# Performance work log

Hardware: AMD Instinct MI355X
Metric: run time of the kernel (lower is better)

## Reference

```python
import jax, jax.numpy as jnp
import numpy as np

N = 20000      # nodes
IN = 256       # in_dim
OUT = 128      # out_dim
S = 8          # num_sect
K = S + 1      # sectors + self branch
EP = 40000     # edges per sector


def setup_inputs() -> dict:
    key = jax.random.key(0)
    ks = jax.random.split(key, 10)
    x = jax.random.normal(ks[0], (N, IN), jnp.float32)
    rows = jax.random.randint(ks[1], (S, EP), 0, N)  # src (adj row)
    cols = jax.random.randint(ks[2], (S, EP), 0, N)  # dst (adj col)
    # degree norms (buffers derived from the graph, as in compute_norm)
    out_deg = np.bincount(np.asarray(rows).ravel(), minlength=N).astype(np.float32)
    in_deg = np.bincount(np.asarray(cols).ravel(), minlength=N).astype(np.float32)
    out_norm = jnp.asarray(np.clip(out_deg, 1.0, None) ** -0.5)[:, None]  # [N,1]
    in_norm = jnp.asarray(np.clip(in_deg, 1.0, None) ** -0.5)[:, None]    # [N,1]
    s = 0.05  # xavier-ish scale
    W_self = jax.random.normal(ks[3], (IN, OUT), jnp.float32) * s
    W_sect = jax.random.normal(ks[4], (S, IN, OUT), jnp.float32) * s
    WC = jax.random.normal(ks[5], (OUT, OUT), jnp.float32) * s
    WD = jax.random.normal(ks[6], (OUT, OUT), jnp.float32) * s
    gate_w = jax.random.normal(ks[7], (2 * K * OUT, 1), jnp.float32) * s
    gate_b = jnp.zeros((1,), jnp.float32)
    return {"x": x, "W_self": W_self, "W_sect": W_sect, "WC": WC, "WD": WD,
            "gate_w": gate_w, "gate_b": gate_b, "out_norm": out_norm,
            "in_norm": in_norm, "rows": rows, "cols": cols}


def reference(x, W_self, W_sect, WC, WD, gate_w, gate_b, out_norm, in_norm, rows, cols):
    n = x.shape[0]
    # --- forward_sector_agg (dropout is identity in eval / drop_rate=0) ---
    z_self = x @ W_self                                    # [N, OUT]
    H = jnp.einsum('ni,sio->sno', x, W_sect) * out_norm    # [S, N, OUT]
    def agg(h, r, c):  # sparse adj @ h : z[src] += h[dst]
        return jax.ops.segment_sum(h[c], r, num_segments=n)
    Z = jax.vmap(agg)(H, rows, cols)                       # [S, N, OUT]
    z = jnp.concatenate([z_self[None], Z], axis=0)         # [K, N, OUT]
    z = jnp.transpose(z, (1, 0, 2)) * in_norm[:, :, None]  # [N, K, OUT]
    # --- heter_sen_interaction ---
    zc = z @ WC                                            # [N, K, D]
    com = jnp.einsum('nkd,njd->nkj', zc, zc)
    ac = jax.nn.softmax(com, axis=2)
    z_com = jnp.einsum('nkj,njd->nkd', ac, zc).reshape(n, -1)
    zd = z @ WD
    sub = zd[:, :, None, :] - zd[:, None, :, :]            # [N, K, K, D]
    ds = jnp.einsum('nkd,nkjd->nkj', zd, sub)
    ad = jax.nn.softmax(ds, axis=2)
    z_dis = jnp.einsum('nkj,nkjd->nkd', ad, sub).reshape(n, -1)
    cat = jnp.concatenate([z_com, z_dis], axis=-1)         # [N, 2*K*D]
    beta = jax.nn.sigmoid(cat @ gate_w + gate_b)           # [N, 1]
    return beta * z_com + (1.0 - beta) * z_dis             # [N, K*D]
```

## Files before the change

### kernel.cpp

```cpp
#include <hip/hip_runtime.h>
#include <math.h>

#define N_NODES 20000
#define IN_DIM  256
#define OUT_DIM 128
#define S_SECT  8
#define K_BR    9
#define NK      (K_BR*OUT_DIM)
#define EP_EDGE 40000
#define N_EDGES (S_SECT*EP_EDGE)
#define N_BINS  (S_SECT*N_NODES)
#define SCAN_BLOCKS 160
#define M_ROWS  (N_NODES*K_BR)
#define BP      264
#define ZP      136

typedef float v4f __attribute__((ext_vector_type(4)));
typedef short v8s __attribute__((ext_vector_type(8)));

__device__ inline unsigned short f2bf(float f) {
  union { float f; unsigned u; } v; v.f = f;
  unsigned r = v.u + 0x7fff + ((v.u >> 16) & 1);
  return (unsigned short)(r >> 16);
}
__device__ inline float bf2f(unsigned short h) {
  union { unsigned u; float f; } v; v.u = ((unsigned)h) << 16;
  return v.f;
}

__global__ __launch_bounds__(256) void k_prep_wt(
    const float* __restrict__ Wself, const float* __restrict__ Wsect,
    unsigned short* __restrict__ Wtg)
{
  const int id = blockIdx.x * 256 + threadIdx.x;
  if (id >= NK*IN_DIM) return;
  const int j = id >> 8, k = id & 255;
  float w;
  if (j < OUT_DIM) w = Wself[(size_t)k*OUT_DIM + j];
  else {
    const int s = (j - OUT_DIM) >> 7, c = (j - OUT_DIM) & 127;
    w = Wsect[(size_t)s*(IN_DIM*OUT_DIM) + (size_t)k*OUT_DIM + c];
  }
  Wtg[id] = f2bf(w);
}

__global__ __launch_bounds__(256) void k_prep_xbf(
    const float* __restrict__ x, unsigned short* __restrict__ xbf)
{
  const int id = blockIdx.x * 256 + threadIdx.x;
  if (id >= N_NODES*IN_DIM/4) return;
  const float4 v = ((const float4*)x)[id];
  uint2 o;
  o.x = (unsigned)f2bf(v.x) | ((unsigned)f2bf(v.y) << 16);
  o.y = (unsigned)f2bf(v.z) | ((unsigned)f2bf(v.w) << 16);
  ((uint2*)xbf)[id] = o;
}

__global__ __launch_bounds__(256, 2) void k_gemm_xw_mfma(
    const unsigned short* __restrict__ xbf, const unsigned short* __restrict__ Wtg,
    const float* __restrict__ outn, const float* __restrict__ inn,
    unsigned short* __restrict__ Hbuf, unsigned short* __restrict__ Zbufh)
{
  __shared__ unsigned short Bls[128*BP];
  const int t = threadIdx.x;
  const int wave = t >> 6, lane = t & 63;
  const int mrow = lane & 15, quad = lane >> 4;
  const int m0 = blockIdx.x * 128 + wave * 32;
  const int jbase = blockIdx.y * 128;

  #pragma unroll
  for (int i = 0; i < 16; ++i) {
    const int idx = t + i*256;
    const int col = idx >> 5, ch = idx & 31;
    *(uint4*)(Bls + col*BP + ch*8) =
        *(const uint4*)(Wtg + (size_t)(jbase + col)*IN_DIM + ch*8);
  }

  v8s afr[2][8];
  #pragma unroll
  for (int rb = 0; rb < 2; ++rb) {
    const int r = m0 + rb*16 + mrow;
    const bool ok = (r < N_NODES);
    const unsigned short* src = xbf + (size_t)r*IN_DIM + quad*8;
    #pragma unroll
    for (int kq = 0; kq < 8; ++kq) {
      v8s f = {0,0,0,0,0,0,0,0};
      if (ok) f = *(const v8s*)(src + kq*32);
      afr[rb][kq] = f;
    }
  }
  __syncthreads();

  v4f acc[2][8];
  #pragma unroll
  for (int rb = 0; rb < 2; ++rb)
    #pragma unroll
    for (int jt = 0; jt < 8; ++jt) acc[rb][jt] = (v4f){0.f,0.f,0.f,0.f};

  #pragma unroll
  for (int kq = 0; kq < 8; ++kq) {
    #pragma unroll
    for (int jt = 0; jt < 8; ++jt) {
      const v8s bf = *(const v8s*)(Bls + (jt*16 + mrow)*BP + kq*32 + quad*8);
      acc[0][jt] = __builtin_amdgcn_mfma_f32_16x16x32_bf16(afr[0][kq], bf, acc[0][jt], 0, 0, 0);
      acc[1][jt] = __builtin_amdgcn_mfma_f32_16x16x32_bf16(afr[1][kq], bf, acc[1][jt], 0, 0, 0);
    }
  }

  if (blockIdx.y == 0) {
    #pragma unroll
    for (int rb = 0; rb < 2; ++rb)
      #pragma unroll
      for (int p = 0; p < 4; ++p) {
        const int R = m0 + rb*16 + quad*4 + p;
        if (R >= N_NODES) continue;
        const float iw = inn[R];
        #pragma unroll
        for (int jt = 0; jt < 8; ++jt)
          Zbufh[(size_t)R*NK + jt*16 + mrow] = f2bf(acc[rb][jt][p] * iw);
      }
  } else {
    const int s = blockIdx.y - 1;
    #pragma unroll
    for (int rb = 0; rb < 2; ++rb)
      #pragma unroll
      for (int p = 0; p < 4; ++p) {
        const int R = m0 + rb*16 + quad*4 + p;
        if (R >= N_NODES) continue;
        const float ow = outn[R];
        #pragma unroll
        for (int jt = 0; jt < 8; ++jt)
          Hbuf[((size_t)s*N_NODES + R)*OUT_DIM + jt*16 + mrow] = f2bf(acc[rb][jt][p] * ow);
      }
  }
}

__global__ __launch_bounds__(256) void k_count(
    const int* __restrict__ rows, int* __restrict__ cnt)
{
  const int id = blockIdx.x * 256 + threadIdx.x;
  if (id >= N_EDGES) return;
  const int s = id / EP_EDGE;
  atomicAdd(&cnt[s * N_NODES + rows[id]], 1);
}

__global__ __launch_bounds__(256) void k_scan1(
    const int* __restrict__ cnt, int* __restrict__ bsum)
{
  __shared__ int sh[256];
  const int t = threadIdx.x;
  const int base = blockIdx.x * 1000;
  int s = 0;
  if (t < 250) {
    const int i = base + t*4;
    s = cnt[i] + cnt[i+1] + cnt[i+2] + cnt[i+3];
  }
  sh[t] = s; __syncthreads();
  for (int off = 128; off > 0; off >>= 1) {
    if (t < off) sh[t] += sh[t + off];
    __syncthreads();
  }
  if (t == 0) bsum[blockIdx.x] = sh[0];
}

__global__ void k_scan2(const int* __restrict__ bsum, int* __restrict__ boff)
{
  if (threadIdx.x == 0) {
    int acc = 0;
    for (int b = 0; b < SCAN_BLOCKS; ++b) { boff[b] = acc; acc += bsum[b]; }
  }
}

__global__ __launch_bounds__(256) void k_scan3(
    const int* __restrict__ cnt, const int* __restrict__ boff,
    int* __restrict__ offs)
{
  __shared__ int sh[256];
  const int t = threadIdx.x;
  const int base = blockIdx.x * 1000;
  int v[4] = {0,0,0,0};
  int mySum = 0;
  if (t < 250) {
    const int i = base + t*4;
    v[0]=cnt[i]; v[1]=cnt[i+1]; v[2]=cnt[i+2]; v[3]=cnt[i+3];
    mySum = v[0]+v[1]+v[2]+v[3];
  }
  sh[t] = mySum; __syncthreads();
  for (int off = 1; off < 256; off <<= 1) {
    int add = (t >= off) ? sh[t - off] : 0;
    __syncthreads();
    sh[t] += add;
    __syncthreads();
  }
  if (t < 250) {
    int excl = boff[blockIdx.x] + sh[t] - mySum;
    const int i = base + t*4;
    offs[i]   = excl;           excl += v[0];
    offs[i+1] = excl;           excl += v[1];
    offs[i+2] = excl;           excl += v[2];
    offs[i+3] = excl;
  }
}

__global__ __launch_bounds__(256) void k_scatter(
    const int* __restrict__ rows, const int* __restrict__ cols,
    const int* __restrict__ offs, int* __restrict__ cur,
    int* __restrict__ eCol)
{
  const int id = blockIdx.x * 256 + threadIdx.x;
  if (id >= N_EDGES) return;
  const int s = id / EP_EDGE;
  const int bin = s * N_NODES + rows[id];
  const int pos = offs[bin] + atomicAdd(&cur[bin], 1);
  eCol[pos] = cols[id];
}

__global__ __launch_bounds__(256) void k_agg_csr(
    const unsigned short* __restrict__ Hbuf, const int* __restrict__ offs,
    const int* __restrict__ cnt, const int* __restrict__ eCol,
    const float* __restrict__ inn, unsigned short* __restrict__ Zbufh)
{
  const long long tid = (long long)blockIdx.x * 256 + threadIdx.x;
  const int group = (int)(tid >> 5);
  if (group >= N_BINS) return;
  const int lane = (int)(tid & 31);
  const int s = group / N_NODES;
  const int r = group - s * N_NODES;
  const int start = offs[group];
  const int n = cnt[group];
  float4 acc = {0.f, 0.f, 0.f, 0.f};
  for (int i = 0; i < n; ++i) {
    const int c = eCol[start + i];
    const uint2 h = *(const uint2*)(Hbuf + ((size_t)s*N_NODES + c)*OUT_DIM + lane*4);
    acc.x += bf2f((unsigned short)h.x);
    acc.y += bf2f((unsigned short)(h.x >> 16));
    acc.z += bf2f((unsigned short)h.y);
    acc.w += bf2f((unsigned short)(h.y >> 16));
  }
  const float w = inn[r];
  uint2 o;
  o.x = (unsigned)f2bf(acc.x * w) | ((unsigned)f2bf(acc.y * w) << 16);
  o.y = (unsigned)f2bf(acc.z * w) | ((unsigned)f2bf(acc.w * w) << 16);
  *(uint2*)(Zbufh + ((size_t)r*K_BR + 1 + s)*OUT_DIM + lane*4) = o;
}

__global__ __launch_bounds__(256) void k_prep_bt(
    const float* __restrict__ WC, const float* __restrict__ WD,
    unsigned short* __restrict__ Btg)
{
  const int id = blockIdx.x * 256 + threadIdx.x;
  const int n = id >> 7, k = id & 127;
  const float w = (n < OUT_DIM) ? WC[k*OUT_DIM + n] : WD[k*OUT_DIM + (n - OUT_DIM)];
  Btg[id] = f2bf(w);
}

__global__ __launch_bounds__(256, 4) void k_gemm_zcd(
    const unsigned short* __restrict__ Zbufh, const unsigned short* __restrict__ Btg,
    unsigned short* __restrict__ ZCD)
{
  __shared__ unsigned short Bls[128*ZP];
  const int t = threadIdx.x;
  const int wave = t >> 6, lane = t & 63;
  const int m0 = blockIdx.x * 128 + wave * 32;
  const int mrow = lane & 15, quad = lane >> 4;

  v8s afr[2][4];
  #pragma unroll
  for (int rb = 0; rb < 2; ++rb) {
    const int r = m0 + rb*16 + mrow;
    const bool ok = (r < M_ROWS);
    const unsigned short* src = Zbufh + (size_t)r*OUT_DIM + quad*8;
    #pragma unroll
    for (int kq = 0; kq < 4; ++kq) {
      v8s f = {0,0,0,0,0,0,0,0};
      if (ok) f = *(const v8s*)(src + kq*32);
      afr[rb][kq] = f;
    }
  }

  for (int jh = 0; jh < 2; ++jh) {
    #pragma unroll
    for (int i = 0; i < 8; ++i) {
      const int idx = t + i*256;
      const int row = idx >> 4, c8 = idx & 15;
      *(uint4*)(Bls + row*ZP + c8*8) =
          *(const uint4*)(Btg + (size_t)(jh*128 + row)*OUT_DIM + c8*8);
    }
    __syncthreads();

    v4f acc[2][8];
    #pragma unroll
    for (int rb = 0; rb < 2; ++rb)
      #pragma unroll
      for (int j = 0; j < 8; ++j) acc[rb][j] = (v4f){0.f,0.f,0.f,0.f};

    #pragma unroll
    for (int j = 0; j < 8; ++j) {
      const unsigned short* bp = Bls + (j*16 + mrow)*ZP + quad*8;
      #pragma unroll
      for (int kq = 0; kq < 4; ++kq) {
        const v8s bf = *(const v8s*)(bp + kq*32);
        acc[0][j] = __builtin_amdgcn_mfma_f32_16x16x32_bf16(afr[0][kq], bf, acc[0][j], 0, 0, 0);
        acc[1][j] = __builtin_amdgcn_mfma_f32_16x16x32_bf16(afr[1][kq], bf, acc[1][j], 0, 0, 0);
      }
    }

    unsigned short* Z = ZCD + (size_t)jh * N_NODES * NK;
    #pragma unroll
    for (int rb = 0; rb < 2; ++rb)
      #pragma unroll
      for (int p = 0; p < 4; ++p) {
        const int R = m0 + rb*16 + quad*4 + p;
        if (R >= M_ROWS) continue;
        const int node = R / 9, kk = R - node*9;
        const size_t base = (size_t)node*NK + kk*OUT_DIM;
        #pragma unroll
        for (int j = 0; j < 8; ++j)
          Z[base + j*16 + mrow] = f2bf(acc[rb][j][p]);
      }
    __syncthreads();
  }
}

__global__ __launch_bounds__(256) void k_gram(
    const unsigned short* __restrict__ ZCD, float* __restrict__ Gbuf)
{
  const int wid = (blockIdx.x * 256 + threadIdx.x) >> 6;
  if (wid >= 2*N_NODES) return;
  const int lane = threadIdx.x & 63;
  const int node = wid >> 1, mat = wid & 1;
  const int r = lane & 15, quad = lane >> 4;

  const unsigned short* src = ZCD + (size_t)mat*N_NODES*NK + (size_t)node*NK
                              + (size_t)r*OUT_DIM + quad*8;
  v8s frag[4];
  #pragma unroll
  for (int kq = 0; kq < 4; ++kq) {
    v8s f = {0,0,0,0,0,0,0,0};
    if (r < K_BR) f = *(const v8s*)(src + kq*32);
    frag[kq] = f;
  }
  v4f acc = {0.f,0.f,0.f,0.f};
  #pragma unroll
  for (int kq = 0; kq < 4; ++kq)
    acc = __builtin_amdgcn_mfma_f32_16x16x32_bf16(frag[kq], frag[kq], acc, 0, 0, 0);

  const int n = lane & 15;
  if (n < K_BR) {
    float* g = Gbuf + ((size_t)node*2 + mat)*81;
    #pragma unroll
    for (int p = 0; p < 4; ++p) {
      const int m = quad*4 + p;
      if (m < K_BR) g[m*9 + n] = acc[p];
    }
  }
}

__global__ __launch_bounds__(256) void k_interact2(
    const unsigned short* __restrict__ ZCD, const float* __restrict__ Gbuf,
    const float* __restrict__ gw, const float* __restrict__ gb,
    float* __restrict__ out)
{
  __shared__ float gs[8][2][K_BR][10];
  __shared__ float redw[2][2];
  const int t  = threadIdx.x;
  const int n0 = blockIdx.x * 8;

  if (t < 144) {
    const int node = t / 18;
    const int rem  = t - node*18;
    const int mat  = (rem >= 9) ? 1 : 0;
    const int k    = rem - mat*9;
    const float* g = Gbuf + ((size_t)(n0+node)*2 + mat)*81 + k*9;
    float v[9];
    if (mat == 0) {
      #pragma unroll
      for (int j = 0; j < 9; ++j) v[j] = g[j];
    } else {
      const float gkk = g[k];
      #pragma unroll
      for (int j = 0; j < 9; ++j) v[j] = gkk - g[j];
    }
    float m = v[0];
    #pragma unroll
    for (int j = 1; j < 9; ++j) m = fmaxf(m, v[j]);
    float sum = 0.f;
    #pragma unroll
    for (int j = 0; j < 9; ++j) { v[j] = expf(v[j] - m); sum += v[j]; }
    const float inv = 1.f / sum;
    #pragma unroll
    for (int j = 0; j < 9; ++j) gs[node][mat][k][j] = v[j] * inv;
  }
  __syncthreads();

  const int half = t >> 7;
  const int d    = t & 127;
  const int wh   = (t >> 6) & 1;
  const int lane = t & 63;
  const float gbv = gb[0];
  float gwc[9], gwd[9];
  #pragma unroll
  for (int j = 0; j < 9; ++j) {
    gwc[j] = gw[j*OUT_DIM + d];
    gwd[j] = gw[NK + j*OUT_DIM + d];
  }

  for (int nn = 0; nn < 4; ++nn) {
    const int node = half*4 + nn;
    const unsigned short* zcp = ZCD + (size_t)(n0+node)*NK + d;
    const unsigned short* zdp = zcp + (size_t)N_NODES*NK;
    float zcj[9], zdj[9];
    #pragma unroll
    for (int j = 0; j < 9; ++j) {
      zcj[j] = bf2f(zcp[j*OUT_DIM]);
      zdj[j] = bf2f(zdp[j*OUT_DIM]);
    }
    float zcomK[9], zdisK[9];
    float gp = 0.f;
    #pragma unroll
    for (int k = 0; k < 9; ++k) {
      float zc = 0.f, ad = 0.f;
      #pragma unroll
      for (int j = 0; j < 9; ++j) {
        zc += gs[node][0][k][j] * zcj[j];
        ad += gs[node][1][k][j] * zdj[j];
      }
      zcomK[k] = zc;
      zdisK[k] = zdj[k] - ad;
      gp += zc * gwc[k] + zdisK[k] * gwd[k];
    }
    #pragma unroll
    for (int off = 32; off > 0; off >>= 1) gp += __shfl_down(gp, off, 64);
    if (lane == 0) redw[half][wh] = gp;
    __syncthreads();
    const float beta = 1.f / (1.f + expf(-(redw[half][0] + redw[half][1] + gbv)));
    #pragma unroll
    for (int k = 0; k < 9; ++k)
      out[(size_t)(n0+node)*NK + k*OUT_DIM + d] = beta*zcomK[k] + (1.f-beta)*zdisK[k];
    __syncthreads();
  }
}

extern "C" void kernel_launch(void* const* d_in, const int* in_sizes, int n_in,
                              void* d_out, int out_size, void* d_ws, size_t ws_size,
                              hipStream_t stream)
{
  const float* x     = (const float*)d_in[0];
  const float* Wself = (const float*)d_in[1];
  const float* Wsect = (const float*)d_in[2];
  const float* WC    = (const float*)d_in[3];
  const float* WD    = (const float*)d_in[4];
  const float* gw    = (const float*)d_in[5];
  const float* gb    = (const float*)d_in[6];
  const float* outn  = (const float*)d_in[7];
  const float* inn   = (const float*)d_in[8];
  const int*   rows  = (const int*)d_in[9];
  const int*   cols  = (const int*)d_in[10];
  float* out = (float*)d_out;

  char* p = (char*)d_ws;
  unsigned short* Hbuf  = (unsigned short*)p; p += (size_t)S_SECT*N_NODES*OUT_DIM*2;
  unsigned short* Zbufh = (unsigned short*)p; p += (size_t)M_ROWS*OUT_DIM*2;
  unsigned short* ZCD   = (unsigned short*)p; p += (size_t)2*N_NODES*NK*2;
  int* cnt    = (int*)p;                      p += (size_t)N_BINS*4;
  int* offs   = (int*)p;                      p += (size_t)N_BINS*4;
  int* cur    = (int*)p;                      p += (size_t)N_BINS*4;
  int* bsum   = (int*)p;                      p += 256*4;
  int* boff   = (int*)p;                      p += 256*4;
  int* eCol   = (int*)p;                      p += (size_t)N_EDGES*4;
  unsigned short* Btg = (unsigned short*)p;   p += 256*128*2;
  unsigned short* Wtg = (unsigned short*)p;   p += (size_t)NK*IN_DIM*2;
  unsigned short* xbf = (unsigned short*)p;   p += (size_t)N_NODES*IN_DIM*2;
  float* Gbuf = (float*)Hbuf;

  hipMemsetAsync(cnt, 0, (size_t)N_BINS*4, stream);
  hipMemsetAsync(cur, 0, (size_t)N_BINS*4, stream);

  k_prep_wt<<<(NK*IN_DIM + 255)/256, 256, 0, stream>>>(Wself, Wsect, Wtg);
  k_prep_bt<<<128, 256, 0, stream>>>(WC, WD, Btg);
  k_prep_xbf<<<(N_NODES*IN_DIM/4 + 255)/256, 256, 0, stream>>>(x, xbf);

  dim3 gA((N_NODES + 127)/128, K_BR);
  k_gemm_xw_mfma<<<gA, 256, 0, stream>>>(xbf, Wtg, outn, inn, Hbuf, Zbufh);

  const int eb = (N_EDGES + 255)/256;
  k_count  <<<eb, 256, 0, stream>>>(rows, cnt);
  k_scan1  <<<SCAN_BLOCKS, 256, 0, stream>>>(cnt, bsum);
  k_scan2  <<<1, 64, 0, stream>>>(bsum, boff);
  k_scan3  <<<SCAN_BLOCKS, 256, 0, stream>>>(cnt, boff, offs);
  k_scatter<<<eb, 256, 0, stream>>>(rows, cols, offs, cur, eCol);

  const int aggBlocks = (N_BINS*32 + 255)/256;
  k_agg_csr<<<aggBlocks, 256, 0, stream>>>(Hbuf, offs, cnt, eCol, inn, Zbufh);

  k_gemm_zcd<<<(M_ROWS + 127)/128, 256, 0, stream>>>(Zbufh, Btg, ZCD);

  k_gram<<<(2*N_NODES)/4, 256, 0, stream>>>(ZCD, Gbuf);

  k_interact2<<<N_NODES/8, 256, 0, stream>>>(ZCD, Gbuf, gw, gb, out);
}
```

Before: 323.9 us.

## Fuse Gram computation into interaction kernel and split X·W GEMM over K halves

```diff
diff --git a/kernel.cpp b/kernel.cpp
--- a/kernel.cpp
+++ b/kernel.cpp
@@ -12,7 +12,6 @@
 #define N_BINS  (S_SECT*N_NODES)
 #define SCAN_BLOCKS 160
 #define M_ROWS  (N_NODES*K_BR)
-#define BP      264
 #define ZP      136
 
 typedef float v4f __attribute__((ext_vector_type(4)));
@@ -56,55 +55,57 @@
   ((uint2*)xbf)[id] = o;
 }
 
-__global__ __launch_bounds__(256, 2) void k_gemm_xw_mfma(
+__global__ __launch_bounds__(256, 4) void k_gemm_xw_mfma(
     const unsigned short* __restrict__ xbf, const unsigned short* __restrict__ Wtg,
     const float* __restrict__ outn, const float* __restrict__ inn,
     unsigned short* __restrict__ Hbuf, unsigned short* __restrict__ Zbufh)
 {
-  __shared__ unsigned short Bls[128*BP];
+  __shared__ unsigned short Bls[128*ZP];
   const int t = threadIdx.x;
   const int wave = t >> 6, lane = t & 63;
   const int mrow = lane & 15, quad = lane >> 4;
   const int m0 = blockIdx.x * 128 + wave * 32;
   const int jbase = blockIdx.y * 128;
 
-  #pragma unroll
-  for (int i = 0; i < 16; ++i) {
-    const int idx = t + i*256;
-    const int col = idx >> 5, ch = idx & 31;
-    *(uint4*)(Bls + col*BP + ch*8) =
-        *(const uint4*)(Wtg + (size_t)(jbase + col)*IN_DIM + ch*8);
-  }
-
-  v8s afr[2][8];
-  #pragma unroll
-  for (int rb = 0; rb < 2; ++rb) {
-    const int r = m0 + rb*16 + mrow;
-    const bool ok = (r < N_NODES);
-    const unsigned short* src = xbf + (size_t)r*IN_DIM + quad*8;
-    #pragma unroll
-    for (int kq = 0; kq < 8; ++kq) {
-      v8s f = {0,0,0,0,0,0,0,0};
-      if (ok) f = *(const v8s*)(src + kq*32);
-      afr[rb][kq] = f;
-    }
-  }
-  __syncthreads();
-
   v4f acc[2][8];
   #pragma unroll
   for (int rb = 0; rb < 2; ++rb)
     #pragma unroll
     for (int jt = 0; jt < 8; ++jt) acc[rb][jt] = (v4f){0.f,0.f,0.f,0.f};
 
-  #pragma unroll
-  for (int kq = 0; kq < 8; ++kq) {
-    #pragma unroll
-    for (int jt = 0; jt < 8; ++jt) {
-      const v8s bf = *(const v8s*)(Bls + (jt*16 + mrow)*BP + kq*32 + quad*8);
-      acc[0][jt] = __builtin_amdgcn_mfma_f32_16x16x32_bf16(afr[0][kq], bf, acc[0][jt], 0, 0, 0);
-      acc[1][jt] = __builtin_amdgcn_mfma_f32_16x16x32_bf16(afr[1][kq], bf, acc[1][jt], 0, 0, 0);
-    }
+  for (int kh = 0; kh < 2; ++kh) {
+    #pragma unroll
+    for (int i = 0; i < 8; ++i) {
+      const int idx = t + i*256;
+      const int row = idx >> 4, c8 = idx & 15;
+      *(uint4*)(Bls + row*ZP + c8*8) =
+          *(const uint4*)(Wtg + (size_t)(jbase + row)*IN_DIM + kh*128 + c8*8);
+    }
+    v8s afr[2][4];
+    #pragma unroll
+    for (int rb = 0; rb < 2; ++rb) {
+      const int r = m0 + rb*16 + mrow;
+      const bool ok = (r < N_NODES);
+      const unsigned short* src = xbf + (size_t)r*IN_DIM + kh*128 + quad*8;
+      #pragma unroll
+      for (int kq = 0; kq < 4; ++kq) {
+        v8s f = {0,0,0,0,0,0,0,0};
+        if (ok) f = *(const v8s*)(src + kq*32);
+        afr[rb][kq] = f;
+      }
+    }
+    __syncthreads();
+
+    #pragma unroll
+    for (int kq = 0; kq < 4; ++kq) {
+      #pragma unroll
+      for (int jt = 0; jt < 8; ++jt) {
+        const v8s bf = *(const v8s*)(Bls + (jt*16 + mrow)*ZP + kq*32 + quad*8);
+        acc[0][jt] = __builtin_amdgcn_mfma_f32_16x16x32_bf16(afr[0][kq], bf, acc[0][jt], 0, 0, 0);
+        acc[1][jt] = __builtin_amdgcn_mfma_f32_16x16x32_bf16(afr[1][kq], bf, acc[1][jt], 0, 0, 0);
+      }
+    }
+    __syncthreads();
   }
 
   if (blockIdx.y == 0) {
@@ -322,64 +323,61 @@
   }
 }
 
-__global__ __launch_bounds__(256) void k_gram(
-    const unsigned short* __restrict__ ZCD, float* __restrict__ Gbuf)
-{
-  const int wid = (blockIdx.x * 256 + threadIdx.x) >> 6;
-  if (wid >= 2*N_NODES) return;
-  const int lane = threadIdx.x & 63;
-  const int node = wid >> 1, mat = wid & 1;
-  const int r = lane & 15, quad = lane >> 4;
-
-  const unsigned short* src = ZCD + (size_t)mat*N_NODES*NK + (size_t)node*NK
-                              + (size_t)r*OUT_DIM + quad*8;
-  v8s frag[4];
-  #pragma unroll
-  for (int kq = 0; kq < 4; ++kq) {
-    v8s f = {0,0,0,0,0,0,0,0};
-    if (r < K_BR) f = *(const v8s*)(src + kq*32);
-    frag[kq] = f;
-  }
-  v4f acc = {0.f,0.f,0.f,0.f};
-  #pragma unroll
-  for (int kq = 0; kq < 4; ++kq)
-    acc = __builtin_amdgcn_mfma_f32_16x16x32_bf16(frag[kq], frag[kq], acc, 0, 0, 0);
-
-  const int n = lane & 15;
-  if (n < K_BR) {
-    float* g = Gbuf + ((size_t)node*2 + mat)*81;
-    #pragma unroll
-    for (int p = 0; p < 4; ++p) {
-      const int m = quad*4 + p;
-      if (m < K_BR) g[m*9 + n] = acc[p];
-    }
-  }
-}
-
-__global__ __launch_bounds__(256) void k_interact2(
-    const unsigned short* __restrict__ ZCD, const float* __restrict__ Gbuf,
+__global__ __launch_bounds__(256) void k_interact3(
+    const unsigned short* __restrict__ ZCD,
     const float* __restrict__ gw, const float* __restrict__ gb,
     float* __restrict__ out)
 {
+  __shared__ float graw[8][2][K_BR][10];
   __shared__ float gs[8][2][K_BR][10];
   __shared__ float redw[2][2];
   const int t  = threadIdx.x;
   const int n0 = blockIdx.x * 8;
+
+  {
+    const int wv = t >> 6, lane = t & 63;
+    const int r = lane & 15, quad = lane >> 4;
+    #pragma unroll
+    for (int q = 0; q < 4; ++q) {
+      const int idx = wv*4 + q;
+      const int node = idx >> 1, mat = idx & 1;
+      const unsigned short* src = ZCD + (size_t)mat*N_NODES*NK
+                                  + (size_t)(n0+node)*NK + (size_t)r*OUT_DIM + quad*8;
+      v8s frag[4];
+      #pragma unroll
+      for (int kq = 0; kq < 4; ++kq) {
+        v8s f = {0,0,0,0,0,0,0,0};
+        if (r < K_BR) f = *(const v8s*)(src + kq*32);
+        frag[kq] = f;
+      }
+      v4f acc = {0.f,0.f,0.f,0.f};
+      #pragma unroll
+      for (int kq = 0; kq < 4; ++kq)
+        acc = __builtin_amdgcn_mfma_f32_16x16x32_bf16(frag[kq], frag[kq], acc, 0, 0, 0);
+      if (r < K_BR) {
+        #pragma unroll
+        for (int p = 0; p < 4; ++p) {
+          const int m = quad*4 + p;
+          if (m < K_BR) graw[node][mat][m][r] = acc[p];
+        }
+      }
+    }
+  }
+  __syncthreads();
 
   if (t < 144) {
     const int node = t / 18;
     const int rem  = t - node*18;
     const int mat  = (rem >= 9) ? 1 : 0;
     const int k    = rem - mat*9;
-    const float* g = Gbuf + ((size_t)(n0+node)*2 + mat)*81 + k*9;
     float v[9];
     if (mat == 0) {
       #pragma unroll
-      for (int j = 0; j < 9; ++j) v[j] = g[j];
+      for (int j = 0; j < 9; ++j) v[j] = graw[node][0][k][j];
     } else {
-      const float gkk = g[k];
-      #pragma unroll
-      for (int j = 0; j < 9; ++j) v[j] = gkk - g[j];
+      const float gkk = graw[node][1][k][k];
+      #pragma unroll
+      for (int j = 0; j < 9; ++j) v[j] = gkk - graw[node][1][k][j];
     }
     float m = v[0];
     #pragma unroll
@@ -471,7 +469,6 @@
   unsigned short* Btg = (unsigned short*)p;   p += 256*128*2;
   unsigned short* Wtg = (unsigned short*)p;   p += (size_t)NK*IN_DIM*2;
   unsigned short* xbf = (unsigned short*)p;   p += (size_t)N_NODES*IN_DIM*2;
-  float* Gbuf = (float*)Hbuf;
 
   hipMemsetAsync(cnt, 0, (size_t)N_BINS*4, stream);
   hipMemsetAsync(cur, 0, (size_t)N_BINS*4, stream);
@@ -495,7 +492,5 @@
 
   k_gemm_zcd<<<(M_ROWS + 127)/128, 256, 0, stream>>>(Zbufh, Btg, ZCD);
 
-  k_gram<<<(2*N_NODES)/4, 256, 0, stream>>>(ZCD, Gbuf);
-
-  k_interact2<<<N_NODES/8, 256, 0, stream>>>(ZCD, Gbuf, gw, gb, out);
-}
+  k_interact3<<<N_NODES/8, 256, 0, stream>>>(ZCD, gw, gb, out);
+}
```

After: 323.2 us. Within noise of the previous version (-0.2%).
